# Kernel optimization log

Measured on AMD Instinct MI355X. Metric: run time of the kernel, lower is better.

## Reference

```python
import jax, jax.numpy as jnp
import numpy as np

N_NODES = 50000
N_EDGES = 800000
N_GRAPHS = 512
IN_DIM = 50
H = 128  # hidden_channels


def _init_linear(key, out_dim, in_dim, bias=True):
    k1, k2 = jax.random.split(key)
    bound = 1.0 / np.sqrt(in_dim)
    W = jax.random.uniform(k1, (out_dim, in_dim), jnp.float32, -bound, bound)
    if bias:
        b = jax.random.uniform(k2, (out_dim,), jnp.float32, -bound, bound)
        return W, b
    return W


def setup_inputs() -> dict:
    key = jax.random.key(0)
    ks = jax.random.split(key, 16)
    x = jax.random.normal(ks[0], (N_NODES, IN_DIM), jnp.float32)
    edge_index = jax.random.randint(ks[1], (2, N_EDGES), 0, N_NODES, jnp.int64)
    batch = jnp.sort(jax.random.randint(ks[2], (N_NODES,), 0, N_GRAPHS, jnp.int64))
    Wl1, bl1 = _init_linear(ks[3], H, IN_DIM)
    Wr1 = _init_linear(ks[4], H, IN_DIM, bias=False)
    Wl2, bl2 = _init_linear(ks[5], 2 * H, H)
    Wr2 = _init_linear(ks[6], 2 * H, H, bias=False)
    Wl3, bl3 = _init_linear(ks[7], 4 * H, 2 * H)
    Wr3 = _init_linear(ks[8], 4 * H, 2 * H, bias=False)
    Wf1, bf1 = _init_linear(ks[9], 2 * H, 4 * H)
    Wf2, bf2 = _init_linear(ks[10], H, 2 * H)
    Wo, bo = _init_linear(ks[11], 1, H)
    return dict(x=x, edge_index=edge_index, batch=batch,
                Wl1=Wl1, bl1=bl1, Wr1=Wr1,
                Wl2=Wl2, bl2=bl2, Wr2=Wr2,
                Wl3=Wl3, bl3=bl3, Wr3=Wr3,
                Wf1=Wf1, bf1=bf1, Wf2=Wf2, bf2=bf2, Wo=Wo, bo=bo)


def sage_conv(x, src, dst, deg_inv, Wl, bl, Wr):
    # mean-aggregate neighbor features at destination nodes, then linear
    agg = jax.ops.segment_sum(x[src], dst, num_segments=N_NODES) * deg_inv
    return agg @ Wl.T + bl + x @ Wr.T


def reference(x, edge_index, batch, Wl1, bl1, Wr1, Wl2, bl2, Wr2,
              Wl3, bl3, Wr3, Wf1, bf1, Wf2, bf2, Wo, bo):
    src, dst = edge_index[0], edge_index[1]
    deg = jax.ops.segment_sum(jnp.ones((N_EDGES,), x.dtype), dst, num_segments=N_NODES)
    deg_inv = (1.0 / jnp.maximum(deg, 1.0))[:, None]

    x1 = jax.nn.leaky_relu(sage_conv(x, src, dst, deg_inv, Wl1, bl1, Wr1))
    x2 = jax.nn.relu(sage_conv(x1, src, dst, deg_inv, Wl2, bl2, Wr2))
    x3 = jax.nn.relu(sage_conv(x2, src, dst, deg_inv, Wl3, bl3, Wr3))

    # global mean pool per graph
    pool_sum = jax.ops.segment_sum(x3, batch, num_segments=N_GRAPHS)
    cnt = jax.ops.segment_sum(jnp.ones((N_NODES,), x.dtype), batch, num_segments=N_GRAPHS)
    x_pool = pool_sum / jnp.maximum(cnt, 1.0)[:, None]

    x4 = jax.nn.relu(x_pool @ Wf1.T + bf1)
    x5 = jax.nn.relu(x4 @ Wf2.T + bf2)
    return jax.nn.sigmoid(x5 @ Wo.T + bo)
```

## Files before the change

kernel.cpp:

```cpp
#include <hip/hip_runtime.h>
#include <math.h>

#define N_NODES 50000
#define N_EDGES 800000
#define N_GRAPHS 512
#define M_PAD 50048
#define SEG_SZ 6250
#define EPT 8
#define SEG_BLOCKS 391
#define COUNT_BLOCKS (SEG_BLOCKS * 8)

typedef unsigned char u8;
typedef unsigned short u16;
typedef unsigned int u32;
typedef long i64;
using floatx4 = __attribute__((ext_vector_type(4))) float;
using floatx2 = __attribute__((ext_vector_type(2))) float;

__device__ __forceinline__ u8 f2fp8(float v) {
    return (u8)(__builtin_amdgcn_cvt_pk_fp8_f32(v, v, 0, false) & 0xFF);
}
__device__ __forceinline__ u32 pack4fp8(float a, float b, float c, float d) {
    u32 p = __builtin_amdgcn_cvt_pk_fp8_f32(a, b, 0, false);
    return __builtin_amdgcn_cvt_pk_fp8_f32(c, d, p, true);
}
__device__ __forceinline__ void acc16fp8(float* acc, uint4 u) {
    const u32 w[4] = {u.x, u.y, u.z, u.w};
    #pragma unroll
    for (int j = 0; j < 4; ++j) {
        floatx2 lo = __builtin_amdgcn_cvt_pk_f32_fp8((int)w[j], false);
        floatx2 hi = __builtin_amdgcn_cvt_pk_f32_fp8((int)w[j], true);
        acc[j * 4 + 0] += lo[0]; acc[j * 4 + 1] += lo[1];
        acc[j * 4 + 2] += hi[0]; acc[j * 4 + 3] += hi[1];
    }
}

__device__ __forceinline__ void load_lds16(const u8* g, u8* l) {
    __builtin_amdgcn_global_load_lds(
        (const __attribute__((address_space(1))) u32*)g,
        (__attribute__((address_space(3))) u32*)l, 16, 0, 0);
}
template<int N> __device__ __forceinline__ void waitcnt_vm() {
    __builtin_amdgcn_s_waitcnt(0x0F70 | N);
}
__device__ __forceinline__ void raw_barrier() {
    asm volatile("s_barrier" ::: "memory");
}

__global__ __launch_bounds__(256) void prep_kernel(
    const int* __restrict__ dst, int* __restrict__ degi,
    const float* __restrict__ x,
    const float* __restrict__ Wl1, const float* __restrict__ Wr1,
    const float* __restrict__ Wl2, const float* __restrict__ Wr2,
    const float* __restrict__ Wl3, const float* __restrict__ Wr3,
    const float* __restrict__ Wf1, const float* __restrict__ Wf2,
    u8* __restrict__ abuf1,
    u8* __restrict__ wb1, u8* __restrict__ wb2, u8* __restrict__ wb3,
    float* __restrict__ Wf1T, float* __restrict__ Wf2T)
{
    if (blockIdx.x < COUNT_BLOCKS) {
        const int bx = blockIdx.x;
        const int seg = bx & 7;
        const int lo = seg * SEG_SZ, hi = lo + SEG_SZ;
        int e = (bx >> 3) * (256 * EPT) + threadIdx.x;
        #pragma unroll
        for (int j = 0; j < EPT; ++j, e += 256) {
            if (e < N_EDGES) {
                int d = dst[e];
                if (d >= lo && d < hi) atomicAdd(&degi[d], 1);
            }
        }
        return;
    }
    int i = (blockIdx.x - COUNT_BLOCKS) * 256 + threadIdx.x;
    if (i < N_NODES * 16) {
        int n = i >> 4, c = (i & 15) * 4;
        float v[4];
        #pragma unroll
        for (int j = 0; j < 4; ++j) {
            int cc = c + j;
            v[j] = (cc < 50) ? x[n * 50 + cc] : 0.0f;
        }
        *(u32*)(abuf1 + (size_t)n * 128 + 64 + c) = pack4fp8(v[0], v[1], v[2], v[3]);
        return;
    }
    i -= N_NODES * 16;
    if (i < 128 * 64) {
        int o = i / 64, c = i % 64;
        float vl = (c < 50) ? Wl1[o * 50 + c] : 0.0f;
        float vr = (c < 50) ? Wr1[o * 50 + c] : 0.0f;
        wb1[(size_t)o * 128 + c] = f2fp8(vl);
        wb1[(size_t)o * 128 + 64 + c] = f2fp8(vr);
        return;
    }
    i -= 128 * 64;
    if (i < 256 * 128) {
        int o = i / 128, c = i % 128;
        wb2[(size_t)o * 256 + c] = f2fp8(Wl2[o * 128 + c]);
        wb2[(size_t)o * 256 + 128 + c] = f2fp8(Wr2[o * 128 + c]);
        return;
    }
    i -= 256 * 128;
    if (i < 512 * 256) {
        int o = i / 256, c = i % 256;
        wb3[(size_t)o * 512 + c] = f2fp8(Wl3[o * 256 + c]);
        wb3[(size_t)o * 512 + 256 + c] = f2fp8(Wr3[o * 256 + c]);
        return;
    }
    i -= 512 * 256;
    if (i < 256 * 512) {
        int o = i >> 9, k = i & 511;
        Wf1T[(size_t)k * 256 + o] = Wf1[(size_t)o * 512 + k];
        return;
    }
    i -= 256 * 512;
    if (i < 128 * 256) {
        int o = i >> 8, k = i & 255;
        Wf2T[(size_t)k * 128 + o] = Wf2[(size_t)o * 256 + k];
    }
}

__global__ void scan1_kernel(const int* __restrict__ degi, int* __restrict__ starts,
                             int* __restrict__ bsum) {
    __shared__ int s[256];
    int t = threadIdx.x, i = blockIdx.x * 256 + t;
    int v = (i < N_NODES) ? degi[i] : 0;
    s[t] = v; __syncthreads();
    for (int off = 1; off < 256; off <<= 1) {
        int x = (t >= off) ? s[t - off] : 0;
        __syncthreads();
        s[t] += x;
        __syncthreads();
    }
    if (i < N_NODES) starts[i] = s[t] - v;
    if (t == 255) bsum[blockIdx.x] = s[255];
}

__global__ void scan2_kernel(const int* __restrict__ bsum, int* __restrict__ boff,
                             int* __restrict__ starts, int nb) {
    __shared__ int s[256];
    int t = threadIdx.x;
    int v = (t < nb) ? bsum[t] : 0;
    s[t] = v; __syncthreads();
    for (int off = 1; off < 256; off <<= 1) {
        int x = (t >= off) ? s[t - off] : 0;
        __syncthreads();
        s[t] += x;
        __syncthreads();
    }
    if (t < nb) boff[t] = s[t] - v;
    if (t == nb - 1) starts[N_NODES] = s[t];
}

__global__ void scan3_gstart_kernel(int* __restrict__ starts, const int* __restrict__ boff,
                                    const int* __restrict__ batch, int* __restrict__ gstart) {
    int i = blockIdx.x * 256 + threadIdx.x;
    if (i >= N_NODES) return;
    starts[i] += boff[blockIdx.x];
    int b = batch[i];
    int bp = (i == 0) ? -1 : batch[i - 1];
    for (int g = bp + 1; g <= b; ++g) gstart[g] = i;
    if (i == N_NODES - 1)
        for (int g = b + 1; g <= N_GRAPHS; ++g) gstart[g] = N_NODES;
}

__global__ __launch_bounds__(256) void fill_seg_kernel(const int* __restrict__ src,
                                                       const int* __restrict__ dst,
                                                       const int* __restrict__ starts,
                                                       int* __restrict__ cursor,
                                                       u16* __restrict__ csr) {
    const int seg = blockIdx.x & 7;
    const int lo = seg * SEG_SZ, hi = lo + SEG_SZ;
    int e = (blockIdx.x >> 3) * (256 * EPT) + threadIdx.x;
    #pragma unroll
    for (int j = 0; j < EPT; ++j, e += 256) {
        if (e < N_EDGES) {
            int d = dst[e];
            if (d >= lo && d < hi) {
                int p = atomicAdd(&cursor[d], 1);
                csr[starts[d] + p] = (u16)src[e];
            }
        }
    }
}

template<int DINP>
__global__ __launch_bounds__(256) void csr_agg_kernel(const int* __restrict__ starts,
                                                      const u16* __restrict__ csr,
                                                      u8* __restrict__ abuf) {
    constexpr int STRIDE = 2 * DINP;
    constexpr int LPR = DINP / 16;
    constexpr int EPW = 64 / LPR;
    const int wave = threadIdx.x >> 6, lane = threadIdx.x & 63;
    const int n = blockIdx.x * 4 + wave;
    if (n >= N_NODES) return;
    const int sub = lane / LPR;
    const int li = lane % LPR;
    const int s0 = starts[n], s1 = starts[n + 1];

    float acc[16] = {};
    const u8* xin = abuf + DINP;

    int e = s0 + sub;
    for (; e + EPW < s1; e += 2 * EPW) {
        int i0 = csr[e], i1 = csr[e + EPW];
        uint4 u0 = *(const uint4*)(xin + (size_t)i0 * STRIDE + li * 16);
        uint4 u1 = *(const uint4*)(xin + (size_t)i1 * STRIDE + li * 16);
        acc16fp8(acc, u0);
        acc16fp8(acc, u1);
    }
    for (; e < s1; e += EPW) {
        int i0 = csr[e];
        uint4 u0 = *(const uint4*)(xin + (size_t)i0 * STRIDE + li * 16);
        acc16fp8(acc, u0);
    }

    #pragma unroll
    for (int off = 32; off >= LPR; off >>= 1) {
        #pragma unroll
        for (int c = 0; c < 16; ++c) acc[c] += __shfl_down(acc[c], off);
    }

    if (lane < LPR) {
        float sc = 1.0f / fmaxf((float)(s1 - s0), 1.0f);
        uint4 o;
        o.x = pack4fp8(acc[0] * sc, acc[1] * sc, acc[2] * sc, acc[3] * sc);
        o.y = pack4fp8(acc[4] * sc, acc[5] * sc, acc[6] * sc, acc[7] * sc);
        o.z = pack4fp8(acc[8] * sc, acc[9] * sc, acc[10] * sc, acc[11] * sc);
        o.w = pack4fp8(acc[12] * sc, acc[13] * sc, acc[14] * sc, acc[15] * sc);
        *(uint4*)(abuf + (size_t)n * STRIDE + li * 16) = o;
    }
}

template<int K, int NB, int ACT>
__global__ __launch_bounds__(256) void gemm_fp8_kernel(
    const u8* __restrict__ A, const u8* __restrict__ W,
    const float* __restrict__ bias,
    u8* __restrict__ out8, int gstride, int goff, int N)
{
    constexpr int NKB = K / 32;
    constexpr int MT = M_PAD / 128;
    constexpr int MCHUNK = (MT + 7) / 8;
    __shared__ __align__(16) u8 As[3][128 * 32];
    __shared__ __align__(16) u8 Bs[3][128 * 32];

    const int bx = blockIdx.x;
    const int xcd = bx & 7;
    const int seq = bx >> 3;
    const int n = seq % NB;
    const int m = xcd * MCHUNK + seq / NB;
    if (m >= MT) return;
    const int bm = m * 128;
    const int bn = n * 128;

    const int tid = threadIdx.x;
    const int wave = tid >> 6, lane = tid & 63;
    const int wm = (wave & 1) * 64, wn = (wave >> 1) * 64;
    const int lm = lane & 15, lq = lane >> 4;

    const int srow = wave * 32 + (lane >> 1);
    const int scol = ((lane & 1) ^ ((lane >> 3) & 1)) * 16;
    const u8* gA = A + (size_t)(bm + srow) * K + scol;
    const u8* gB = W + (size_t)(bn + srow) * K + scol;
    const int lbase = wave * 32 * 32;

    auto stage = [&](int s, int r) {
        const int ko = s * 32;
        load_lds16(gA + ko, &As[r][lbase]);
        load_lds16(gB + ko, &Bs[r][lbase]);
    };

    floatx4 acc[4][4] = {};

    stage(0, 0);
    stage(1, 1);

    const int csw = (((lq >> 1) ^ ((lm >> 2) & 1)) << 4) + (lq & 1) * 8;

    #pragma unroll
    for (int kb = 0; kb < NKB; ++kb) {
        if (kb + 2 < NKB) stage(kb + 2, (kb + 2) % 3);
        const int rem = NKB - 1 - kb;
        if (rem >= 2)      waitcnt_vm<4>();
        else if (rem == 1) waitcnt_vm<2>();
        else               waitcnt_vm<0>();
        raw_barrier();

        const int r = kb % 3;
        i64 af[4], bfr[4];
        #pragma unroll
        for (int mi = 0; mi < 4; ++mi)
            af[mi] = *(const i64*)&As[r][(wm + mi * 16 + lm) * 32 + csw];
        #pragma unroll
        for (int ni = 0; ni < 4; ++ni)
            bfr[ni] = *(const i64*)&Bs[r][(wn + ni * 16 + lm) * 32 + csw];
        #pragma unroll
        for (int mi = 0; mi < 4; ++mi)
            #pragma unroll
            for (int ni = 0; ni < 4; ++ni)
                acc[mi][ni] = __builtin_amdgcn_mfma_f32_16x16x32_fp8_fp8(
                    af[mi], bfr[ni], acc[mi][ni], 0, 0, 0);
        raw_barrier();
    }

    #pragma unroll
    for (int mi = 0; mi < 4; ++mi) {
        int node0 = bm + wm + mi * 16 + lq * 4;
        #pragma unroll
        for (int ni = 0; ni < 4; ++ni) {
            int o = bn + wn + ni * 16 + lm;
            float bi = bias[o];
            #pragma unroll
            for (int r = 0; r < 4; ++r) {
                int node = node0 + r;
                if (node >= N) continue;
                float v = acc[mi][ni][r] + bi;
                if (ACT == 0) v = (v > 0.0f) ? v : 0.01f * v;
                else          v = fmaxf(v, 0.0f);
                out8[(size_t)node * gstride + goff + o] = f2fp8(v);
            }
        }
    }
}

__global__ __launch_bounds__(256) void pool_kernel(
    const u8* __restrict__ x3, const int* __restrict__ gstart,
    float* __restrict__ pool)
{
    __shared__ float sacc[32][128];
    const int g = blockIdx.x >> 2;
    const int slab = blockIdx.x & 3;
    const int t = threadIdx.x;
    const int chain = t >> 3;
    const int li = t & 7;
    const int c0 = slab * 128 + li * 16;
    const int n0 = gstart[g], n1 = gstart[g + 1];

    float acc[16] = {};
    for (int n = n0 + chain; n < n1; n += 32) {
        uint4 u = *(const uint4*)(x3 + (size_t)n * 512 + c0);
        acc16fp8(acc, u);
    }
    #pragma unroll
    for (int j = 0; j < 16; ++j) sacc[chain][li * 16 + j] = acc[j];
    __syncthreads();
    if (t < 128) {
        float s = 0.0f;
        #pragma unroll
        for (int r = 0; r < 32; ++r) s += sacc[r][t];
        pool[(size_t)g * 512 + slab * 128 + t] = s;
    }
}

__global__ __launch_bounds__(256) void dense_head_kernel(
    const float* __restrict__ pool, const int* __restrict__ gstart,
    const float* __restrict__ Wf1T, const float* __restrict__ bf1,
    const float* __restrict__ Wf2T, const float* __restrict__ bf2,
    const float* __restrict__ Wo,  const float* __restrict__ bo,
    float* __restrict__ out)
{
    __shared__ float sp[512];
    __shared__ float s4[256];
    __shared__ float red[128];
    const int g = blockIdx.x;
    const int t = threadIdx.x;
    const float sc = 1.0f / fmaxf((float)(gstart[g + 1] - gstart[g]), 1.0f);

    sp[t]       = pool[(size_t)g * 512 + t] * sc;
    sp[t + 256] = pool[(size_t)g * 512 + 256 + t] * sc;
    __syncthreads();

    {
        float s = bf1[t];
        #pragma unroll 8
        for (int k = 0; k < 512; ++k) s += sp[k] * Wf1T[(size_t)k * 256 + t];
        s4[t] = fmaxf(s, 0.0f);
    }
    __syncthreads();
    if (t < 128) {
        float s = bf2[t];
        #pragma unroll 8
        for (int k = 0; k < 256; ++k) s += s4[k] * Wf2T[(size_t)k * 128 + t];
        red[t] = fmaxf(s, 0.0f) * Wo[t];
    }
    __syncthreads();
    for (int off = 64; off >= 1; off >>= 1) {
        if (t < off) red[t] += red[t + off];
        __syncthreads();
    }
    if (t == 0) out[g] = 1.0f / (1.0f + expf(-(red[0] + bo[0])));
}

extern "C" void kernel_launch(void* const* d_in, const int* in_sizes, int n_in,
                              void* d_out, int out_size, void* d_ws, size_t ws_size,
                              hipStream_t stream)
{
    const float* x     = (const float*)d_in[0];
    const int*   ei    = (const int*)  d_in[1];
    const int*   batch = (const int*)  d_in[2];
    const float* Wl1   = (const float*)d_in[3];
    const float* bl1   = (const float*)d_in[4];
    const float* Wr1   = (const float*)d_in[5];
    const float* Wl2   = (const float*)d_in[6];
    const float* bl2   = (const float*)d_in[7];
    const float* Wr2   = (const float*)d_in[8];
    const float* Wl3   = (const float*)d_in[9];
    const float* bl3   = (const float*)d_in[10];
    const float* Wr3   = (const float*)d_in[11];
    const float* Wf1   = (const float*)d_in[12];
    const float* bf1   = (const float*)d_in[13];
    const float* Wf2   = (const float*)d_in[14];
    const float* bf2   = (const float*)d_in[15];
    const float* Wo    = (const float*)d_in[16];
    const float* bo    = (const float*)d_in[17];

    const int* src = ei;
    const int* dst = ei + N_EDGES;

    char* p = (char*)d_ws;
    auto alloc = [&](size_t bytes) { char* r = p; p += (bytes + 255) & ~(size_t)255; return r; };
    int*   gstart = (int*)  alloc(513 * 4);
    float* pool   = (float*)alloc((size_t)512 * 512 * 4);
    float* Wf1T   = (float*)alloc((size_t)512 * 256 * 4);
    float* Wf2T   = (float*)alloc((size_t)256 * 128 * 4);
    u8*    abuf1  = (u8*)   alloc((size_t)M_PAD * 128);
    u8*    abuf2  = (u8*)   alloc((size_t)M_PAD * 256);
    u8*    abuf3  = (u8*)   alloc((size_t)M_PAD * 512);
    u8*    x3buf8 = (u8*)   alloc((size_t)M_PAD * 512);
    u8*    wb1    = (u8*)   alloc((size_t)128 * 128);
    u8*    wb2    = (u8*)   alloc((size_t)256 * 256);
    u8*    wb3    = (u8*)   alloc((size_t)512 * 512);
    char*  zbase  = p;
    int*   degi   = (int*)  alloc(50176 * 4);
    int*   cursor = (int*)  alloc(50176 * 4);
    size_t zbytes = (size_t)(p - zbase);
    int*   starts = (int*)  alloc(50432 * 4);
    int*   bsum   = (int*)  alloc(256 * 4);
    int*   boff   = (int*)  alloc(256 * 4);
    u16*   csr    = (u16*)  alloc((size_t)N_EDGES * 2);

    hipMemsetAsync(zbase, 0, zbytes, stream);
    const int CONV_N = N_NODES * 16 + 128 * 64 + 256 * 128 + 512 * 256
                     + 256 * 512 + 128 * 256;
    const int CONV_BLOCKS = (CONV_N + 255) / 256;
    prep_kernel<<<COUNT_BLOCKS + CONV_BLOCKS, 256, 0, stream>>>(
        dst, degi, x, Wl1, Wr1, Wl2, Wr2, Wl3, Wr3, Wf1, Wf2,
        abuf1, wb1, wb2, wb3, Wf1T, Wf2T);
    scan1_kernel<<<196, 256, 0, stream>>>(degi, starts, bsum);
    scan2_kernel<<<1, 256, 0, stream>>>(bsum, boff, starts, 196);
    scan3_gstart_kernel<<<196, 256, 0, stream>>>(starts, boff, batch, gstart);
    fill_seg_kernel<<<SEG_BLOCKS * 8, 256, 0, stream>>>(src, dst, starts, cursor, csr);

    const int GB = 12500;
    const int GEMM_GRID = 49 * 8;

    csr_agg_kernel<64><<<GB, 256, 0, stream>>>(starts, csr, abuf1);
    gemm_fp8_kernel<128, 1, 0><<<GEMM_GRID * 1, 256, 0, stream>>>(
        abuf1, wb1, bl1, abuf2, 256, 128, N_NODES);

    csr_agg_kernel<128><<<GB, 256, 0, stream>>>(starts, csr, abuf2);
    gemm_fp8_kernel<256, 2, 1><<<GEMM_GRID * 2, 256, 0, stream>>>(
        abuf2, wb2, bl2, abuf3, 512, 256, N_NODES);

    csr_agg_kernel<256><<<GB, 256, 0, stream>>>(starts, csr, abuf3);
    gemm_fp8_kernel<512, 4, 1><<<GEMM_GRID * 4, 256, 0, stream>>>(
        abuf3, wb3, bl3, x3buf8, 512, 0, N_NODES);

    pool_kernel<<<N_GRAPHS * 4, 256, 0, stream>>>(x3buf8, gstart, pool);
    dense_head_kernel<<<N_GRAPHS, 256, 0, stream>>>(
        pool, gstart, Wf1T, bf1, Wf2T, bf2, Wo, bo, (float*)d_out);
}
```

Measured before the change: 374.4 us.

## Add 256x256-tile 8-wave FP8 GEMM with triple-buffered LDS for layers 2 and 3

Adds a new GEMM kernel that uses 512 threads, 256x256 output tiles, a three-stage LDS ring filled by direct global-to-LDS loads, and four barrier-separated MFMA phases that interleave the next tile's loads with compute and raise wave priority during MFMA. Layers 2 and 3 switch to this kernel, and M_PAD grows so the row count is a multiple of 256. The larger tiles are meant to improve operand reuse and hide memory latency. In exchange the grid is much smaller and each block uses more registers and LDS, which may lower occupancy.

New measurement: 431.2 us. 1.15x slower.

```diff
diff --git a/kernel.cpp b/kernel.cpp
--- a/kernel.cpp
+++ b/kernel.cpp
@@ -4,7 +4,7 @@
 #define N_NODES 50000
 #define N_EDGES 800000
 #define N_GRAPHS 512
-#define M_PAD 50048
+#define M_PAD 50176
 #define SEG_SZ 6250
 #define EPT 8
 #define SEG_BLOCKS 391
@@ -314,6 +314,116 @@
             for (int r = 0; r < 4; ++r) {
                 int node = node0 + r;
                 if (node >= N) continue;
+                float v = acc[mi][ni][r] + bi;
+                if (ACT == 0) v = (v > 0.0f) ? v : 0.01f * v;
+                else          v = fmaxf(v, 0.0f);
+                out8[(size_t)node * gstride + goff + o] = f2fp8(v);
+            }
+        }
+    }
+}
+
+template<int MH, int NH, int SS, bool DW, int NK, typename F>
+__device__ __forceinline__ void gphase(const u8* asrc, const u8* bsrc, int cA,
+                                       floatx4 (&acc)[8][4], int t, F&& stage)
+{
+    i64 af[4][2], bv[2][2];
+    #pragma unroll
+    for (int mi = 0; mi < 4; ++mi)
+        #pragma unroll
+        for (int ks = 0; ks < 2; ++ks)
+            af[mi][ks] = *(const i64*)(asrc + (MH * 4 + mi) * 1024 + (cA ^ (ks * 32)));
+    #pragma unroll
+    for (int ni = 0; ni < 2; ++ni)
+        #pragma unroll
+        for (int ks = 0; ks < 2; ++ks)
+            bv[ni][ks] = *(const i64*)(bsrc + (NH * 2 + ni) * 1024 + (cA ^ (ks * 32)));
+
+    if constexpr (SS >= 0) { if (t + 2 < NK) stage(t + 2, SS); }
+    if constexpr (DW) {
+        if (t + 2 < NK) waitcnt_vm<4>();
+        else            waitcnt_vm<0>();
+    }
+    __builtin_amdgcn_s_barrier();
+    asm volatile("s_waitcnt lgkmcnt(0)" ::: "memory");
+    __builtin_amdgcn_sched_barrier(0);
+    __builtin_amdgcn_s_setprio(1);
+    #pragma unroll
+    for (int mi = 0; mi < 4; ++mi)
+        #pragma unroll
+        for (int ni = 0; ni < 2; ++ni)
+            #pragma unroll
+            for (int ks = 0; ks < 2; ++ks)
+                acc[MH * 4 + mi][NH * 2 + ni] =
+                    __builtin_amdgcn_mfma_f32_16x16x32_fp8_fp8(
+                        af[mi][ks], bv[ni][ks],
+                        acc[MH * 4 + mi][NH * 2 + ni], 0, 0, 0);
+    __builtin_amdgcn_s_setprio(0);
+    __builtin_amdgcn_s_barrier();
+}
+
+template<int K, int NB, int ACT>
+__global__ __launch_bounds__(512, 2) void gemm8_fp8_kernel(
+    const u8* __restrict__ A, const u8* __restrict__ W,
+    const float* __restrict__ bias,
+    u8* __restrict__ out8, int gstride, int goff)
+{
+    constexpr int NK = K / 64;
+    __shared__ __align__(16) u8 As[3][256 * 64];
+    __shared__ __align__(16) u8 Bs[3][256 * 64];
+
+    const int bx = blockIdx.x;
+    const int m = (NB == 1) ? bx : (bx >> 1);
+    const int n = (NB == 1) ? 0  : (bx & 1);
+    const int bm = m * 256, bn = n * 256;
+
+    const int tid  = threadIdx.x;
+    const int wave = tid >> 6, lane = tid & 63;
+    const int lm = lane & 15, lq = lane >> 4;
+    const int wr = wave >> 2, wc = wave & 3;
+
+    const int srow = tid >> 2;
+    const int scd  = ((tid & 3) << 4) ^ ((srow & 3) << 4);
+    const u8* gA0 = A + (size_t)(bm + srow) * K + scd;
+    const u8* gB0 = W + (size_t)(bn + srow) * K + scd;
+
+    auto stage = [&](int kt, int s) {
+        const int b = kt % 3;
+        const size_t so = (size_t)kt * 64 + (s ? (size_t)128 * K : (size_t)0);
+        load_lds16(gA0 + so, &As[b][wave * 1024 + s * 8192]);
+        load_lds16(gB0 + so, &Bs[b][wave * 1024 + s * 8192]);
+    };
+
+    floatx4 acc[8][4] = {};
+
+    stage(0, 0); stage(0, 1); stage(1, 0); stage(1, 1);
+    waitcnt_vm<4>();
+    __builtin_amdgcn_s_barrier();
+
+    const int arow_base = (wr * 128 + lm) * 64;
+    const int brow_base = (wc * 64 + lm) * 64;
+    const int cA = (lq << 3) ^ ((lm & 3) << 4);
+
+    for (int t = 0; t < NK; ++t) {
+        const u8* asrc = &As[t % 3][arow_base];
+        const u8* bsrc = &Bs[t % 3][brow_base];
+        gphase<0, 0,  0, false, NK>(asrc, bsrc, cA, acc, t, stage);
+        gphase<0, 1,  1, false, NK>(asrc, bsrc, cA, acc, t, stage);
+        gphase<1, 0, -1, false, NK>(asrc, bsrc, cA, acc, t, stage);
+        gphase<1, 1, -1, true,  NK>(asrc, bsrc, cA, acc, t, stage);
+    }
+
+    #pragma unroll
+    for (int mi = 0; mi < 8; ++mi) {
+        const int node0 = bm + wr * 128 + mi * 16 + lq * 4;
+        #pragma unroll
+        for (int ni = 0; ni < 4; ++ni) {
+            const int o = bn + wc * 64 + ni * 16 + lm;
+            const float bi = bias[o];
+            #pragma unroll
+            for (int r = 0; r < 4; ++r) {
+                const int node = node0 + r;
+                if (node >= N_NODES) continue;
                 float v = acc[mi][ni][r] + bi;
                 if (ACT == 0) v = (v > 0.0f) ? v : 0.01f * v;
                 else          v = fmaxf(v, 0.0f);
@@ -455,16 +565,16 @@
     const int GEMM_GRID = 49 * 8;
 
     csr_agg_kernel<64><<<GB, 256, 0, stream>>>(starts, csr, abuf1);
-    gemm_fp8_kernel<128, 1, 0><<<GEMM_GRID * 1, 256, 0, stream>>>(
+    gemm_fp8_kernel<128, 1, 0><<<GEMM_GRID, 256, 0, stream>>>(
         abuf1, wb1, bl1, abuf2, 256, 128, N_NODES);
 
     csr_agg_kernel<128><<<GB, 256, 0, stream>>>(starts, csr, abuf2);
-    gemm_fp8_kernel<256, 2, 1><<<GEMM_GRID * 2, 256, 0, stream>>>(
-        abuf2, wb2, bl2, abuf3, 512, 256, N_NODES);
+    gemm8_fp8_kernel<256, 1, 1><<<M_PAD / 256, 512, 0, stream>>>(
+        abuf2, wb2, bl2, abuf3, 512, 256);
 
     csr_agg_kernel<256><<<GB, 256, 0, stream>>>(starts, csr, abuf3);
-    gemm_fp8_kernel<512, 4, 1><<<GEMM_GRID * 4, 256, 0, stream>>>(
-        abuf3, wb3, bl3, x3buf8, 512, 0, N_NODES);
+    gemm8_fp8_kernel<512, 2, 1><<<(M_PAD / 256) * 2, 512, 0, stream>>>(
+        abuf3, wb3, bl3, x3buf8, 512, 0);
 
     pool_kernel<<<N_GRAPHS * 4, 256, 0, stream>>>(x3buf8, gstart, pool);
     dense_head_kernel<<<N_GRAPHS, 256, 0, stream>>>(
```
